# Performance work log

Hardware: AMD Instinct MI355X
Metric: run time of the kernel (lower is better)

Reference implementation:

```python
import jax, jax.numpy as jnp
import numpy as np

# Config constants from the module
E = 64    # n_routed_experts
K = 6     # num_experts_per_tok
D = 128   # hidden_size
M = 80    # moe_intermediate_size
MS = 160  # shared expert intermediate = moe_intermediate_size * n_shared_experts
B, S = 64, 256

def _init_w(k, shape, fan_in):
    # kaiming_uniform(a=sqrt(5)) used by nn.Linear / MoEGate: bound = 1/sqrt(fan_in)
    bound = 1.0 / np.sqrt(fan_in)
    return jax.random.uniform(k, shape, jnp.float32, -bound, bound)

def setup_inputs() -> dict:
    key = jax.random.key(0)
    ks = jax.random.split(key, 8)
    return {
        "hidden_states": jax.random.normal(ks[0], (B, S, D), jnp.float32),
        "gate_w": _init_w(ks[1], (E, D), D),        # MoEGate.linear.weight [E, gating_dim]
        "wg": _init_w(ks[2], (E, D, M), D),          # stacked expert gate_proj (transposed)
        "wu": _init_w(ks[3], (E, D, M), D),          # stacked expert up_proj
        "wd": _init_w(ks[4], (E, M, D), M),          # stacked expert down_proj
        "swg": _init_w(ks[5], (D, MS), D),           # shared expert gate_proj
        "swu": _init_w(ks[6], (D, MS), D),           # shared expert up_proj
        "swd": _init_w(ks[7], (MS, D), MS),          # shared expert down_proj
    }

def reference(hidden_states, gate_w, wg, wu, wd, swg, swu, swd):
    orig_shape = hidden_states.shape
    x = hidden_states.reshape(-1, D)                       # [T, D] flat tokens
    T = x.shape[0]
    # --- MoEGate ('all_agent' mode): softmax scoring + top-k + renorm ---
    scores = jax.nn.softmax(x @ gate_w.T, axis=-1)          # [T, E]
    topk_w, topk_idx = jax.lax.top_k(scores, K)             # [T, K]
    topk_w = topk_w / (jnp.sum(topk_w, axis=-1, keepdims=True) + 1e-20)
    # Scatter top-k weights into dense per-expert combine weights [T, E]
    cw = jnp.zeros_like(scores).at[jnp.arange(T)[:, None], topk_idx].add(topk_w)
    # --- Routed experts: SiLU-gated MLP per expert, combined by cw ---
    g = jax.nn.silu(jnp.einsum('td,edm->tem', x, wg)) * jnp.einsum('td,edm->tem', x, wu)
    y = jnp.einsum('tem,emd,te->td', g, wd, cw)             # down-proj + weighted combine
    # --- Shared experts ---
    shared = (jax.nn.silu(x @ swg) * (x @ swu)) @ swd       # [T, D]
    return (y + shared).reshape(orig_shape)
```

## Files before the change

### kernel.cpp

```cpp
#include <hip/hip_runtime.h>
#include <hip/hip_bf16.h>
#include <math.h>


typedef unsigned short ushort_t;
typedef __attribute__((ext_vector_type(8))) short bf16x8;
typedef __attribute__((ext_vector_type(4))) float f32x4;

#define EALL  66

#define OFF_TOPKI 16384
#define OFF_WORK  409600
#define OFF_TOPKW 802816
#define OFF_PERM  1196032
#define OFF_PERMW 1589248
#define OFF_POS2  1982464
#define OFF_YPERM 2375680
#define OFF_YSH   27541504
#define OFF_WGT   31735808
#define OFF_WUT   33087488
#define OFF_WDP   34439168
#define OFF_XB    36061184
#define OFF_HIST  40255488
#define OFF_BOFF  40321024
#define NEED_FAST 40386560
#define FOFF_YBUF 2375680
#define FOFF_WGT  10764288
#define FOFF_WUT  12115968
#define FOFF_WDP  13467648
#define FOFF_XB   15089664
#define FOFF_HIST 19283968
#define FOFF_BOFF 19349504

__device__ __forceinline__ float bf2f(ushort_t u) {
    unsigned int x = ((unsigned int)u) << 16;
    float f; __builtin_memcpy(&f, &x, 4); return f;
}
__device__ __forceinline__ ushort_t f2bf(float f) {
    unsigned int x; __builtin_memcpy(&x, &f, 4);
    unsigned int r = (x + 0x7fffu + ((x >> 16) & 1u)) >> 16;
    return (ushort_t)r;
}
__device__ __forceinline__ float ldin(const void* p, int i, int f32m) {
    return f32m ? ((const float*)p)[i] : bf2f(((const ushort_t*)p)[i]);
}
__device__ __forceinline__ int detect_f32m(const ushort_t* gw) {
    int lane = threadIdx.x & 63;
    int cnt = 0;
    #pragma unroll
    for (int j = 0; j < 4; ++j) {
        ushort_t u = gw[lane * 4 + j];
        if (((u >> 7) & 0xFF) >= 0x7C) cnt++;
    }
    #pragma unroll
    for (int off = 32; off; off >>= 1) cnt += __shfl_xor(cnt, off);
    return (cnt >= 8) ? 1 : 0;
}
__device__ __forceinline__ void gl16(void* l, const void* g) {
    __builtin_amdgcn_global_load_lds(
        (const __attribute__((address_space(1))) void*)g,
        (__attribute__((address_space(3))) void*)l, 16, 0, 0);
}

__global__ __launch_bounds__(1024) void k_pg(const void* x, const void* gw,
        const void* wg, const void* wu, const void* wd,
        const void* swg, const void* swu, const void* swd,
        ushort_t* wgT, ushort_t* wuT, ushort_t* wdP,
        ushort_t* xB, int* topk_i, float* topk_w, int* histPart) {
    __shared__ __align__(16) char smem[41984];
    int tid = threadIdx.x, bid = blockIdx.x;
    int f32m = detect_f32m((const ushort_t*)gw);

    if (bid < 3 * EALL) {
        float* lds = (float*)smem;
        int mat = bid / EALL, e = bid % EALL;
        if (mat < 2) {
            const void* src  = (mat == 0) ? wg  : wu;
            const void* ssrc = (mat == 0) ? swg : swu;
            for (int i = tid; i < 10240; i += 1024) {
                int d = i / 80, m = i % 80;
                float v = (e < 64) ? ldin(src, e * 10240 + i, f32m)
                                   : ldin(ssrc, d * 160 + (e - 64) * 80 + m, f32m);
                lds[d * 81 + m] = v;
            }
            __syncthreads();
            ushort_t* dst = ((mat == 0) ? wgT : wuT) + e * 10240;
            for (int o = tid; o < 10240; o += 1024) {
                int m = o >> 7, d = o & 127;
                dst[o] = f2bf(lds[d * 81 + m]);
            }
        } else {
            for (int i = tid; i < 10240; i += 1024) {
                float v = (e < 64) ? ldin(wd, e * 10240 + i, f32m)
                                   : ldin(swd, (e - 64) * 10240 + i, f32m);
                int m = i >> 7, d = i & 127;
                lds[m * 129 + d] = v;
            }
            __syncthreads();
            ushort_t* dst = wdP + e * 12288;
            for (int o = tid; o < 12288; o += 1024) {
                int d = o / 96, m = o % 96;
                dst[o] = (m < 80) ? f2bf(lds[m * 129 + d]) : (ushort_t)0;
            }
        }
        return;
    }

    float* gwl  = (float*)smem;
    float (*xl)[128] = (float(*)[128])(smem + 33280);
    int*   histL = (int*)(smem + 41472);
    int b = bid - 3 * EALL;
    for (int i = tid; i < 8192; i += 1024)
        gwl[(i >> 7) * 130 + (i & 127)] = ldin(gw, i, f32m);
    if (tid < 64) histL[tid] = 0;
    __syncthreads();
    int wv = tid >> 6, lane = tid & 63;
    for (int q = 0; q < 4; ++q) {
        int t = b * 64 + wv * 4 + q;
        float xv0, xv1;
        if (f32m) {
            float2 v = ((const float2*)((const float*)x + t * 128))[lane];
            xv0 = v.x; xv1 = v.y;
        } else {
            unsigned int pr = *(const unsigned int*)((const ushort_t*)x + t * 128 + lane * 2);
            xv0 = bf2f((ushort_t)(pr & 0xffffu));
            xv1 = bf2f((ushort_t)(pr >> 16));
        }
        float2 xw; xw.x = xv0; xw.y = xv1;
        *(float2*)&xl[wv][lane * 2] = xw;
        unsigned int packed = (unsigned int)f2bf(xv0) | ((unsigned int)f2bf(xv1) << 16);
        *(unsigned int*)(xB + t * 128 + lane * 2) = packed;
        float acc = 0.f;
        #pragma unroll
        for (int d2 = 0; d2 < 64; ++d2) {
            float2 xv = *(const float2*)&xl[wv][d2 * 2];
            float2 gv = *(const float2*)&gwl[lane * 130 + d2 * 2];
            acc = fmaf(xv.x, gv.x, acc);
            acc = fmaf(xv.y, gv.y, acc);
        }
        float mx = acc;
        #pragma unroll
        for (int off = 32; off; off >>= 1) mx = fmaxf(mx, __shfl_xor(mx, off));
        float p = expf(acc - mx);
        float sm = p;
        #pragma unroll
        for (int off = 32; off; off >>= 1) sm += __shfl_xor(sm, off);
        float sc = p / sm;
        float cur = sc;
        float wk6[6]; int ik[6];
        #pragma unroll
        for (int k = 0; k < 6; ++k) {
            float bv = cur; int bi = lane;
            #pragma unroll
            for (int off = 1; off < 64; off <<= 1) {
                float ov = __shfl_xor(bv, off); int oi = __shfl_xor(bi, off);
                if (ov > bv || (ov == bv && oi < bi)) { bv = ov; bi = oi; }
            }
            wk6[k] = bv; ik[k] = bi;
            if (lane == bi) cur = -INFINITY;
        }
        if (lane == 0) {
            float den = wk6[0] + wk6[1] + wk6[2] + wk6[3] + wk6[4] + wk6[5] + 1e-20f;
            #pragma unroll
            for (int k = 0; k < 6; ++k) {
                topk_i[t * 6 + k] = ik[k];
                topk_w[t * 6 + k] = wk6[k] / den;
                atomicAdd(&histL[ik[k]], 1);
            }
        }
    }
    __syncthreads();
    if (tid < 64) histPart[tid * 256 + b] = histL[tid];
}

__global__ __launch_bounds__(256) void k_scan(int* Wi, const int* histPart,
        int* boffG, int* wk) {
    __shared__ int hl[16384];
    __shared__ int cntL[64], exclL[64], chxL[65];
    int tid = threadIdx.x, lane = tid & 63, wv = tid >> 6;
    for (int j = tid; j < 16384; j += 256) hl[j] = histPart[j];
    __syncthreads();
    for (int ei = 0; ei < 16; ++ei) {
        int e = wv * 16 + ei;
        int carry = 0;
        for (int r = 0; r < 4; ++r) {
            int v = hl[e * 256 + r * 64 + lane];
            int incl = v;
            #pragma unroll
            for (int off = 1; off < 64; off <<= 1) {
                int ts = __shfl_up(incl, off);
                if (lane >= off) incl += ts;
            }
            hl[e * 256 + r * 64 + lane] = carry + incl - v;
            carry += __shfl(incl, 63);
        }
        if (lane == 0) cntL[e] = carry;
    }
    __syncthreads();
    if (tid == 0) {
        int s = 0, cs = 0;
        for (int e = 0; e < 64; ++e) {
            exclL[e] = s; s += cntL[e];
            chxL[e] = cs; cs += (cntL[e] + 127) >> 7;
        }
        chxL[64] = cs;
        Wi[128] = s;
        Wi[193] = cs + 256;
    }
    __syncthreads();
    if (tid < 64) { Wi[tid] = cntL[tid]; Wi[64 + tid] = exclL[tid]; }
    for (int j = tid; j < 16384; j += 256) boffG[j] = hl[j] + exclL[j >> 8];
    wk[tid] = (64 << 16) | tid;
    if (tid < 64) {
        int e = tid, nc = (cntL[e] + 127) >> 7, bb = chxL[e];
        for (int c = 0; c < nc; ++c) wk[256 + bb + c] = (e << 16) | c;
    }
}

__global__ __launch_bounds__(256) void k_scatter(const int* topk_i, const float* topk_w,
        const int* boffG, int* perm, float* permw, int* pos2) {
    __shared__ int lcur[64];
    int tid = threadIdx.x, b = blockIdx.x;
    if (tid < 64) lcur[tid] = boffG[tid * 256 + b];
    __syncthreads();
    for (int i = tid; i < 384; i += 256) {
        int g = b * 384 + i;
        int e = topk_i[g];
        float w = topk_w[g];
        int p = atomicAdd(&lcur[e], 1);
        perm[p]  = b * 64 + i / 6;
        permw[p] = w;
        pos2[g]  = p;
    }
}

template<int FAST>
__global__ __launch_bounds__(256) void k_expert(const ushort_t* x, const ushort_t* wgT,
        const ushort_t* wuT, const ushort_t* wdP, const int* Wi, const int* wk,
        const int* perm, const float* permw, ushort_t* yperm, ushort_t* ysh, float* ybuf) {
    __shared__ __align__(16) char hl[32768];
    __shared__ __align__(16) char bufA[20480];
    __shared__ __align__(16) char bufB[20480];

    if (blockIdx.x >= Wi[193]) return;
    int entry = wk[blockIdx.x];
    int e = entry >> 16, c = entry & 0xffff;
    int tid = threadIdx.x, lid = tid & 63, wv = tid >> 6;
    int kg  = (lid >> 4) * 16;
    int kq8 = (lid >> 4) * 8;

    if (e < 64) {
        int n = Wi[e], base = Wi[64 + e];
        int nrows = n - c * 128; if (nrows > 128) nrows = 128;

        {
            const ushort_t* gS = wgT + e * 10240;
            const ushort_t* uS = wuT + e * 10240;
            #pragma unroll
            for (int i = 0; i < 5; ++i) {
                int s = wv * 320 + i * 64 + lid;
                int row = s >> 4, sc = (s & 15) ^ (row & 7);
                gl16(bufA + wv * 5120 + i * 1024, gS + row * 128 + sc * 8);
                gl16(bufB + wv * 5120 + i * 1024, uS + row * 128 + sc * 8);
            }
        }
        bf16x8 a[2][4];
        #pragma unroll
        for (int tr = 0; tr < 2; ++tr) {
            int arow = wv * 32 + tr * 16 + (lid & 15);
            int r = (arow < nrows) ? arow : (nrows - 1);
            int t = perm[base + c * 128 + r];
            #pragma unroll
            for (int k = 0; k < 4; ++k)
                a[tr][k] = *(const bf16x8*)(x + t * 128 + k * 32 + kq8);
        }
        __syncthreads();

        #pragma unroll
        for (int mi = 0; mi < 5; ++mi) {
            int brow = mi * 16 + (lid & 15);
            int bro = brow * 256, bsw = (brow & 7) << 4;
            f32x4 ag[2], au[2];
            #pragma unroll
            for (int tr = 0; tr < 2; ++tr) {
                ag[tr] = (f32x4){0.f, 0.f, 0.f, 0.f};
                au[tr] = (f32x4){0.f, 0.f, 0.f, 0.f};
            }
            #pragma unroll
            for (int k = 0; k < 4; ++k) {
                int bo = bro + (((k * 64) + kg) ^ bsw);
                bf16x8 bg = *(const bf16x8*)(bufA + bo);
                bf16x8 bu = *(const bf16x8*)(bufB + bo);
                #pragma unroll
                for (int tr = 0; tr < 2; ++tr) {
                    ag[tr] = __builtin_amdgcn_mfma_f32_16x16x32_bf16(a[tr][k], bg, ag[tr], 0, 0, 0);
                    au[tr] = __builtin_amdgcn_mfma_f32_16x16x32_bf16(a[tr][k], bu, au[tr], 0, 0, 0);
                }
            }
            #pragma unroll
            for (int tr = 0; tr < 2; ++tr) {
                #pragma unroll
                for (int rg = 0; rg < 4; ++rg) {
                    float g = ag[tr][rg], uu2 = au[tr][rg];
                    float h = (g / (1.f + __expf(-g))) * uu2;
                    int row = wv * 32 + tr * 16 + (lid >> 4) * 4 + rg;
                    int cb = (mi * 16 + (lid & 15)) * 2;
                    *(ushort_t*)(hl + row * 256 + (cb ^ ((row & 7) << 4))) = f2bf(h);
                }
            }
        }
        {
            int r = wv * 32 + (lid >> 1), ch = 10 + (lid & 1);
            uint4 z = {0u, 0u, 0u, 0u};
            *(uint4*)(hl + r * 256 + ((ch * 16) ^ ((r & 7) << 4))) = z;
        }
        __syncthreads();

        {
            const ushort_t* dS = wdP + e * 12288;
            #pragma unroll
            for (int i = 0; i < 4; ++i) {
                int s = wv * 256 + i * 64 + lid;
                int r = s >> 4, sc = (s & 15) ^ (r & 7);
                int off = (sc < 12) ? sc * 8 : 0;
                gl16(bufA + wv * 4096 + i * 1024, dS + r * 96 + off);
                gl16(bufB + wv * 4096 + i * 1024, dS + (64 + r) * 96 + off);
            }
        }
        __syncthreads();

        bf16x8 bfr[2][3];
        #pragma unroll
        for (int tf = 0; tf < 2; ++tf) {
            int brow = wv * 32 + tf * 16 + (lid & 15);
            #pragma unroll
            for (int k = 0; k < 3; ++k)
                bfr[tf][k] = *(const bf16x8*)(hl + brow * 256 + (((k * 64) + kg) ^ ((brow & 7) << 4)));
        }
        f32x4 acc[8][2];
        #pragma unroll
        for (int dt = 0; dt < 8; ++dt) {
            acc[dt][0] = (f32x4){0.f, 0.f, 0.f, 0.f};
            acc[dt][1] = (f32x4){0.f, 0.f, 0.f, 0.f};
        }
        #pragma unroll
        for (int dt = 0; dt < 8; ++dt) {
            int r = (dt & 3) * 16 + (lid & 15);
            const char* wb = (dt < 4) ? bufA : bufB;
            bf16x8 ad[3];
            #pragma unroll
            for (int k = 0; k < 3; ++k)
                ad[k] = *(const bf16x8*)(wb + r * 256 + (((k * 64) + kg) ^ ((r & 7) << 4)));
            #pragma unroll
            for (int tf = 0; tf < 2; ++tf) {
                f32x4 cc = acc[dt][tf];
                #pragma unroll
                for (int k = 0; k < 3; ++k)
                    cc = __builtin_amdgcn_mfma_f32_16x16x32_bf16(ad[k], bfr[tf][k], cc, 0, 0, 0);
                acc[dt][tf] = cc;
            }
        }

        #pragma unroll
        for (int tf = 0; tf < 2; ++tf) {
            int rloc = wv * 32 + tf * 16 + (lid & 15);
            int rc = (rloc < nrows) ? rloc : (nrows - 1);
            float w = FAST ? permw[base + c * 128 + rc] : 0.f;
            #pragma unroll
            for (int dt = 0; dt < 8; ++dt) {
                if (FAST) {
                    int cb = (dt * 16 + (lid >> 4) * 4) * 2;
                    ushort_t o[4];
                    #pragma unroll
                    for (int rg = 0; rg < 4; ++rg) o[rg] = f2bf(acc[dt][tf][rg] * w);
                    *(uint2*)(hl + rloc * 256 + (cb ^ ((rloc & 7) << 4))) = *(const uint2*)o;
                } else {
                    if (rloc < nrows) {
                        int t = perm[base + c * 128 + rloc];
                        float w2 = permw[base + c * 128 + rloc];
                        int d0 = dt * 16 + (lid >> 4) * 4;
                        #pragma unroll
                        for (int rg = 0; rg < 4; ++rg)
                            atomicAdd(&ybuf[t * 128 + d0 + rg], acc[dt][tf][rg] * w2);
                    }
                }
            }
        }
        if (FAST) {
            #pragma unroll
            for (int ps = 0; ps < 8; ++ps) {
                int row = wv * 32 + ps * 4 + (lid >> 4);
                int cb = (lid & 15) * 16;
                uint4 v = *(const uint4*)(hl + row * 256 + (cb ^ ((row & 7) << 4)));
                if (row < nrows)
                    *(uint4*)(yperm + (size_t)(base + c * 128 + row) * 128 + (lid & 15) * 8) = v;
            }
        }
    } else {
        bf16x8 a1[4];
        int arow = wv * 16 + (lid & 15);
        int t0 = c * 64 + arow;
        #pragma unroll
        for (int k = 0; k < 4; ++k)
            a1[k] = *(const bf16x8*)(x + t0 * 128 + k * 32 + kq8);

        f32x4 acc[8];
        #pragma unroll
        for (int dt = 0; dt < 8; ++dt) acc[dt] = (f32x4){0.f, 0.f, 0.f, 0.f};

        for (int sub = 0; sub < 2; ++sub) {
            int ee = 64 + sub;
            {
                const ushort_t* gS = wgT + ee * 10240;
                const ushort_t* uS = wuT + ee * 10240;
                #pragma unroll
                for (int i = 0; i < 5; ++i) {
                    int s = wv * 320 + i * 64 + lid;
                    int row = s >> 4, sc = (s & 15) ^ (row & 7);
                    gl16(bufA + wv * 5120 + i * 1024, gS + row * 128 + sc * 8);
                    gl16(bufB + wv * 5120 + i * 1024, uS + row * 128 + sc * 8);
                }
            }
            __syncthreads();
            #pragma unroll
            for (int mi = 0; mi < 5; ++mi) {
                int brow = mi * 16 + (lid & 15);
                int bro = brow * 256, bsw = (brow & 7) << 4;
                f32x4 ag = {0.f, 0.f, 0.f, 0.f};
                f32x4 au = {0.f, 0.f, 0.f, 0.f};
                #pragma unroll
                for (int k = 0; k < 4; ++k) {
                    int bo = bro + (((k * 64) + kg) ^ bsw);
                    bf16x8 bg = *(const bf16x8*)(bufA + bo);
                    bf16x8 bu = *(const bf16x8*)(bufB + bo);
                    ag = __builtin_amdgcn_mfma_f32_16x16x32_bf16(a1[k], bg, ag, 0, 0, 0);
                    au = __builtin_amdgcn_mfma_f32_16x16x32_bf16(a1[k], bu, au, 0, 0, 0);
                }
                #pragma unroll
                for (int rg = 0; rg < 4; ++rg) {
                    float g = ag[rg], uu2 = au[rg];
                    float h = (g / (1.f + __expf(-g))) * uu2;
                    int row = wv * 16 + (lid >> 4) * 4 + rg;
                    int cb = (mi * 16 + (lid & 15)) * 2;
                    *(ushort_t*)(hl + row * 256 + (cb ^ ((row & 7) << 4))) = f2bf(h);
                }
            }
            if (sub == 0 && lid < 32) {
                int r = wv * 16 + (lid >> 1), ch = 10 + (lid & 1);
                uint4 z = {0u, 0u, 0u, 0u};
                *(uint4*)(hl + r * 256 + ((ch * 16) ^ ((r & 7) << 4))) = z;
            }
            __syncthreads();
            {
                const ushort_t* dS = wdP + ee * 12288;
                #pragma unroll
                for (int i = 0; i < 4; ++i) {
                    int s = wv * 256 + i * 64 + lid;
                    int r = s >> 4, sc = (s & 15) ^ (r & 7);
                    int off = (sc < 12) ? sc * 8 : 0;
                    gl16(bufA + wv * 4096 + i * 1024, dS + r * 96 + off);
                    gl16(bufB + wv * 4096 + i * 1024, dS + (64 + r) * 96 + off);
                }
            }
            __syncthreads();
            int brow = wv * 16 + (lid & 15);
            #pragma unroll
            for (int dt = 0; dt < 8; ++dt) {
                int r = (dt & 3) * 16 + (lid & 15);
                const char* wb = (dt < 4) ? bufA : bufB;
                bf16x8 ad[3];
                #pragma unroll
                for (int k = 0; k < 3; ++k)
                    ad[k] = *(const bf16x8*)(wb + r * 256 + (((k * 64) + kg) ^ ((r & 7) << 4)));
                f32x4 cc = acc[dt];
                #pragma unroll
                for (int k = 0; k < 3; ++k) {
                    bf16x8 b = *(const bf16x8*)(hl + brow * 256 + (((k * 64) + kg) ^ ((brow & 7) << 4)));
                    cc = __builtin_amdgcn_mfma_f32_16x16x32_bf16(ad[k], b, cc, 0, 0, 0);
                }
                acc[dt] = cc;
            }
            __syncthreads();
        }

        int rloc = wv * 16 + (lid & 15);
        if (FAST) {
            #pragma unroll
            for (int dt = 0; dt < 8; ++dt) {
                int cb = (dt * 16 + (lid >> 4) * 4) * 2;
                ushort_t o[4];
                #pragma unroll
                for (int rg = 0; rg < 4; ++rg) o[rg] = f2bf(acc[dt][rg]);
                *(uint2*)(hl + rloc * 256 + (cb ^ ((rloc & 7) << 4))) = *(const uint2*)o;
            }
            #pragma unroll
            for (int ps = 0; ps < 4; ++ps) {
                int row = wv * 16 + ps * 4 + (lid >> 4);
                int cb = (lid & 15) * 16;
                uint4 v = *(const uint4*)(hl + row * 256 + (cb ^ ((row & 7) << 4)));
                *(uint4*)(ysh + (size_t)(c * 64 + row) * 128 + (lid & 15) * 8) = v;
            }
        } else {
            int t = c * 64 + rloc;
            #pragma unroll
            for (int dt = 0; dt < 8; ++dt) {
                int d0 = dt * 16 + (lid >> 4) * 4;
                #pragma unroll
                for (int rg = 0; rg < 4; ++rg)
                    atomicAdd(&ybuf[t * 128 + d0 + rg], acc[dt][rg]);
            }
        }
    }
}

__global__ __launch_bounds__(256) void k_final_gather(const ushort_t* yperm,
        const ushort_t* ysh, const int* pos2, void* out, const ushort_t* gwDet) {
    int idx = blockIdx.x * 256 + threadIdx.x;
    int t = idx >> 4, cg = (idx & 15) * 8;
    int f32m = detect_f32m(gwDet);
    float acc[8];
    {
        uint4 v = *(const uint4*)(ysh + (size_t)t * 128 + cg);
        const ushort_t* u = (const ushort_t*)&v;
        #pragma unroll
        for (int j = 0; j < 8; ++j) acc[j] = bf2f(u[j]);
    }
    const int* pp = pos2 + t * 6;
    #pragma unroll
    for (int k = 0; k < 6; ++k) {
        int p = pp[k];
        uint4 v = *(const uint4*)(yperm + (size_t)p * 128 + cg);
        const ushort_t* u = (const ushort_t*)&v;
        #pragma unroll
        for (int j = 0; j < 8; ++j) acc[j] += bf2f(u[j]);
    }
    if (f32m) {
        float4 o0 = {acc[0], acc[1], acc[2], acc[3]};
        float4 o1 = {acc[4], acc[5], acc[6], acc[7]};
        float* op = (float*)out + (size_t)t * 128 + cg;
        *(float4*)op = o0; *(float4*)(op + 4) = o1;
    } else {
        ushort_t o[8];
        #pragma unroll
        for (int j = 0; j < 8; ++j) o[j] = f2bf(acc[j]);
        *(uint4*)((ushort_t*)out + (size_t)t * 128 + cg) = *(const uint4*)o;
    }
}

__global__ __launch_bounds__(256) void k_final_ybuf(const float* ybuf, void* out,
        const ushort_t* gwDet) {
    int i = blockIdx.x * 256 + threadIdx.x;
    int f32m = detect_f32m(gwDet);
    float4 v = ((const float4*)ybuf)[i];
    if (f32m) {
        ((float4*)out)[i] = v;
    } else {
        ushort4 o;
        o.x = f2bf(v.x); o.y = f2bf(v.y); o.z = f2bf(v.z); o.w = f2bf(v.w);
        ((ushort4*)out)[i] = o;
    }
}

extern "C" void kernel_launch(void* const* d_in, const int* in_sizes, int n_in,
                              void* d_out, int out_size, void* d_ws, size_t ws_size,
                              hipStream_t stream) {
    (void)in_sizes; (void)n_in; (void)out_size;
    const void* x   = d_in[0];
    const void* gw  = d_in[1];
    const void* wg  = d_in[2];
    const void* wu  = d_in[3];
    const void* wd  = d_in[4];
    const void* swg = d_in[5];
    const void* swu = d_in[6];
    const void* swd = d_in[7];

    char* ws = (char*)d_ws;
    int fast = (ws_size >= (size_t)NEED_FAST) ? 1 : 0;

    int*      Wi     = (int*)d_ws;
    int*      topk_i = (int*)(ws + OFF_TOPKI);
    int*      wklist = (int*)(ws + OFF_WORK);
    float*    topk_w = (float*)(ws + OFF_TOPKW);
    int*      perm   = (int*)(ws + OFF_PERM);
    float*    permw  = (float*)(ws + OFF_PERMW);
    int*      pos2   = (int*)(ws + OFF_POS2);

    ushort_t* yperm = (ushort_t*)(ws + OFF_YPERM);
    ushort_t* ysh   = (ushort_t*)(ws + OFF_YSH);
    float*    ybuf  = (float*)(ws + FOFF_YBUF);
    ushort_t* wgT   = (ushort_t*)(ws + (fast ? OFF_WGT  : FOFF_WGT));
    ushort_t* wuT   = (ushort_t*)(ws + (fast ? OFF_WUT  : FOFF_WUT));
    ushort_t* wdP   = (ushort_t*)(ws + (fast ? OFF_WDP  : FOFF_WDP));
    ushort_t* xB    = (ushort_t*)(ws + (fast ? OFF_XB   : FOFF_XB));
    int*      histP = (int*)(ws + (fast ? OFF_HIST : FOFF_HIST));
    int*      boffG = (int*)(ws + (fast ? OFF_BOFF : FOFF_BOFF));

    if (!fast) hipMemsetAsync(ybuf, 0, 16384 * 128 * 4, stream);

    k_pg<<<3 * EALL + 256, 1024, 0, stream>>>(x, gw, wg, wu, wd, swg, swu, swd,
                                              wgT, wuT, wdP, xB, topk_i, topk_w, histP);
    k_scan<<<1, 256, 0, stream>>>(Wi, histP, boffG, wklist);
    k_scatter<<<256, 256, 0, stream>>>(topk_i, topk_w, boffG, perm, permw, pos2);
    if (fast) {
        k_expert<1><<<1088, 256, 0, stream>>>(xB, wgT, wuT, wdP, Wi, wklist, perm, permw, yperm, ysh, ybuf);
        k_final_gather<<<1024, 256, 0, stream>>>(yperm, ysh, pos2, d_out, (const ushort_t*)gw);
    } else {
        k_expert<0><<<1088, 256, 0, stream>>>(xB, wgT, wuT, wdP, Wi, wklist, perm, permw, yperm, ysh, ybuf);
        k_final_ybuf<<<2048, 256, 0, stream>>>(ybuf, d_out, (const ushort_t*)gw);
    }
}
```

Baseline: 92.65 us.

## Fuse shared-expert compute into scatter kernel, shrink routed-expert grid

The shared-expert MLP blocks move out of the routed expert kernel into a new kernel that also performs the token scatter. Blocks 0-255 do the scatter and blocks 256-511 compute shared-expert chunks, so that independent work fills one launch and the expert kernel loses its per-block branch. The routed-expert grid drops to 896 blocks and the work list no longer reserves shared-expert entries. The risk is that 896 may not cover the worst-case number of routed chunks.

```diff
diff --git a/kernel.cpp b/kernel.cpp
--- a/kernel.cpp
+++ b/kernel.cpp
@@ -205,39 +205,169 @@
         }
         chxL[64] = cs;
         Wi[128] = s;
-        Wi[193] = cs + 256;
+        Wi[193] = cs;
     }
     __syncthreads();
     if (tid < 64) { Wi[tid] = cntL[tid]; Wi[64 + tid] = exclL[tid]; }
     for (int j = tid; j < 16384; j += 256) boffG[j] = hl[j] + exclL[j >> 8];
-    wk[tid] = (64 << 16) | tid;
     if (tid < 64) {
         int e = tid, nc = (cntL[e] + 127) >> 7, bb = chxL[e];
-        for (int c = 0; c < nc; ++c) wk[256 + bb + c] = (e << 16) | c;
-    }
-}
-
-__global__ __launch_bounds__(256) void k_scatter(const int* topk_i, const float* topk_w,
-        const int* boffG, int* perm, float* permw, int* pos2) {
-    __shared__ int lcur[64];
-    int tid = threadIdx.x, b = blockIdx.x;
-    if (tid < 64) lcur[tid] = boffG[tid * 256 + b];
-    __syncthreads();
-    for (int i = tid; i < 384; i += 256) {
-        int g = b * 384 + i;
-        int e = topk_i[g];
-        float w = topk_w[g];
-        int p = atomicAdd(&lcur[e], 1);
-        perm[p]  = b * 64 + i / 6;
-        permw[p] = w;
-        pos2[g]  = p;
+        for (int c = 0; c < nc; ++c) wk[bb + c] = (e << 16) | c;
+    }
+}
+
+template<int FAST>
+__global__ __launch_bounds__(256) void k_sc_sh(const int* boffG,
+        const int* topk_i, const float* topk_w, int* perm, float* permw, int* pos2,
+        const ushort_t* x, const ushort_t* wgT, const ushort_t* wuT, const ushort_t* wdP,
+        ushort_t* ysh, float* ybuf) {
+    __shared__ __align__(16) char smem[73728];
+    int tid = threadIdx.x, lid = tid & 63, wv = tid >> 6;
+    int bid = blockIdx.x;
+
+    if (bid < 256) {
+        int* lcur = (int*)smem;
+        int b = bid;
+        if (tid < 64) lcur[tid] = boffG[tid * 256 + b];
+        __syncthreads();
+        for (int i = tid; i < 384; i += 256) {
+            int g = b * 384 + i;
+            int e = topk_i[g];
+            float w = topk_w[g];
+            int p = atomicAdd(&lcur[e], 1);
+            perm[p]  = b * 64 + i / 6;
+            permw[p] = w;
+            pos2[g]  = p;
+        }
+        return;
+    }
+
+    char* hl   = smem;
+    char* bufA = smem + 32768;
+    char* bufB = smem + 53248;
+    int c = bid - 256;
+    int kg  = (lid >> 4) * 16;
+    int kq8 = (lid >> 4) * 8;
+
+    bf16x8 a1[4];
+    int arow = wv * 16 + (lid & 15);
+    int t0 = c * 64 + arow;
+    #pragma unroll
+    for (int k = 0; k < 4; ++k)
+        a1[k] = *(const bf16x8*)(x + t0 * 128 + k * 32 + kq8);
+
+    f32x4 acc[8];
+    #pragma unroll
+    for (int dt = 0; dt < 8; ++dt) acc[dt] = (f32x4){0.f, 0.f, 0.f, 0.f};
+
+    for (int sub = 0; sub < 2; ++sub) {
+        int ee = 64 + sub;
+        {
+            const ushort_t* gS = wgT + ee * 10240;
+            const ushort_t* uS = wuT + ee * 10240;
+            #pragma unroll
+            for (int i = 0; i < 5; ++i) {
+                int s = wv * 320 + i * 64 + lid;
+                int row = s >> 4, sc = (s & 15) ^ (row & 7);
+                gl16(bufA + wv * 5120 + i * 1024, gS + row * 128 + sc * 8);
+                gl16(bufB + wv * 5120 + i * 1024, uS + row * 128 + sc * 8);
+            }
+        }
+        __syncthreads();
+        #pragma unroll
+        for (int mi = 0; mi < 5; ++mi) {
+            int brow = mi * 16 + (lid & 15);
+            int bro = brow * 256, bsw = (brow & 7) << 4;
+            f32x4 ag = {0.f, 0.f, 0.f, 0.f};
+            f32x4 au = {0.f, 0.f, 0.f, 0.f};
+            #pragma unroll
+            for (int k = 0; k < 4; ++k) {
+                int bo = bro + (((k * 64) + kg) ^ bsw);
+                bf16x8 bg = *(const bf16x8*)(bufA + bo);
+                bf16x8 bu = *(const bf16x8*)(bufB + bo);
+                ag = __builtin_amdgcn_mfma_f32_16x16x32_bf16(a1[k], bg, ag, 0, 0, 0);
+                au = __builtin_amdgcn_mfma_f32_16x16x32_bf16(a1[k], bu, au, 0, 0, 0);
+            }
+            #pragma unroll
+            for (int rg = 0; rg < 4; ++rg) {
+                float g = ag[rg], uu2 = au[rg];
+                float h = (g / (1.f + __expf(-g))) * uu2;
+                int row = wv * 16 + (lid >> 4) * 4 + rg;
+                int cb = (mi * 16 + (lid & 15)) * 2;
+                *(ushort_t*)(hl + row * 256 + (cb ^ ((row & 7) << 4))) = f2bf(h);
+            }
+        }
+        if (sub == 0 && lid < 32) {
+            int r = wv * 16 + (lid >> 1), ch = 10 + (lid & 1);
+            uint4 z = {0u, 0u, 0u, 0u};
+            *(uint4*)(hl + r * 256 + ((ch * 16) ^ ((r & 7) << 4))) = z;
+        }
+        __syncthreads();
+        {
+            const ushort_t* dS = wdP + ee * 12288;
+            #pragma unroll
+            for (int i = 0; i < 4; ++i) {
+                int s = wv * 256 + i * 64 + lid;
+                int r = s >> 4, sc = (s & 15) ^ (r & 7);
+                int off = (sc < 12) ? sc * 8 : 0;
+                gl16(bufA + wv * 4096 + i * 1024, dS + r * 96 + off);
+                gl16(bufB + wv * 4096 + i * 1024, dS + (64 + r) * 96 + off);
+            }
+        }
+        __syncthreads();
+        int brow = wv * 16 + (lid & 15);
+        #pragma unroll
+        for (int dt = 0; dt < 8; ++dt) {
+            int r = (dt & 3) * 16 + (lid & 15);
+            const char* wb = (dt < 4) ? bufA : bufB;
+            bf16x8 ad[3];
+            #pragma unroll
+            for (int k = 0; k < 3; ++k)
+                ad[k] = *(const bf16x8*)(wb + r * 256 + (((k * 64) + kg) ^ ((r & 7) << 4)));
+            f32x4 cc = acc[dt];
+            #pragma unroll
+            for (int k = 0; k < 3; ++k) {
+                bf16x8 b = *(const bf16x8*)(hl + brow * 256 + (((k * 64) + kg) ^ ((brow & 7) << 4)));
+                cc = __builtin_amdgcn_mfma_f32_16x16x32_bf16(ad[k], b, cc, 0, 0, 0);
+            }
+            acc[dt] = cc;
+        }
+        __syncthreads();
+    }
+
+    int rloc = wv * 16 + (lid & 15);
+    if (FAST) {
+        #pragma unroll
+        for (int dt = 0; dt < 8; ++dt) {
+            int cb = (dt * 16 + (lid >> 4) * 4) * 2;
+            ushort_t o[4];
+            #pragma unroll
+            for (int rg = 0; rg < 4; ++rg) o[rg] = f2bf(acc[dt][rg]);
+            *(uint2*)(hl + rloc * 256 + (cb ^ ((rloc & 7) << 4))) = *(const uint2*)o;
+        }
+        #pragma unroll
+        for (int ps = 0; ps < 4; ++ps) {
+            int row = wv * 16 + ps * 4 + (lid >> 4);
+            int cb = (lid & 15) * 16;
+            uint4 v = *(const uint4*)(hl + row * 256 + (cb ^ ((row & 7) << 4)));
+            *(uint4*)(ysh + (size_t)(c * 64 + row) * 128 + (lid & 15) * 8) = v;
+        }
+    } else {
+        int t = c * 64 + rloc;
+        #pragma unroll
+        for (int dt = 0; dt < 8; ++dt) {
+            int d0 = dt * 16 + (lid >> 4) * 4;
+            #pragma unroll
+            for (int rg = 0; rg < 4; ++rg)
+                atomicAdd(&ybuf[t * 128 + d0 + rg], acc[dt][rg]);
+        }
     }
 }
 
 template<int FAST>
 __global__ __launch_bounds__(256) void k_expert(const ushort_t* x, const ushort_t* wgT,
         const ushort_t* wuT, const ushort_t* wdP, const int* Wi, const int* wk,
-        const int* perm, const float* permw, ushort_t* yperm, ushort_t* ysh, float* ybuf) {
+        const int* perm, const float* permw, ushort_t* yperm, float* ybuf) {
     __shared__ __align__(16) char hl[32768];
     __shared__ __align__(16) char bufA[20480];
     __shared__ __align__(16) char bufB[20480];
@@ -249,266 +379,150 @@
     int kg  = (lid >> 4) * 16;
     int kq8 = (lid >> 4) * 8;
 
-    if (e < 64) {
-        int n = Wi[e], base = Wi[64 + e];
-        int nrows = n - c * 128; if (nrows > 128) nrows = 128;
-
-        {
-            const ushort_t* gS = wgT + e * 10240;
-            const ushort_t* uS = wuT + e * 10240;
-            #pragma unroll
-            for (int i = 0; i < 5; ++i) {
-                int s = wv * 320 + i * 64 + lid;
-                int row = s >> 4, sc = (s & 15) ^ (row & 7);
-                gl16(bufA + wv * 5120 + i * 1024, gS + row * 128 + sc * 8);
-                gl16(bufB + wv * 5120 + i * 1024, uS + row * 128 + sc * 8);
-            }
-        }
-        bf16x8 a[2][4];
+    int n = Wi[e], base = Wi[64 + e];
+    int nrows = n - c * 128; if (nrows > 128) nrows = 128;
+
+    {
+        const ushort_t* gS = wgT + e * 10240;
+        const ushort_t* uS = wuT + e * 10240;
+        #pragma unroll
+        for (int i = 0; i < 5; ++i) {
+            int s = wv * 320 + i * 64 + lid;
+            int row = s >> 4, sc = (s & 15) ^ (row & 7);
+            gl16(bufA + wv * 5120 + i * 1024, gS + row * 128 + sc * 8);
+            gl16(bufB + wv * 5120 + i * 1024, uS + row * 128 + sc * 8);
+        }
+    }
+    bf16x8 a[2][4];
+    #pragma unroll
+    for (int tr = 0; tr < 2; ++tr) {
+        int arow = wv * 32 + tr * 16 + (lid & 15);
+        int r = (arow < nrows) ? arow : (nrows - 1);
+        int t = perm[base + c * 128 + r];
+        #pragma unroll
+        for (int k = 0; k < 4; ++k)
+            a[tr][k] = *(const bf16x8*)(x + t * 128 + k * 32 + kq8);
+    }
+    __syncthreads();
+
+    #pragma unroll
+    for (int mi = 0; mi < 5; ++mi) {
+        int brow = mi * 16 + (lid & 15);
+        int bro = brow * 256, bsw = (brow & 7) << 4;
+        f32x4 ag[2], au[2];
         #pragma unroll
         for (int tr = 0; tr < 2; ++tr) {
-            int arow = wv * 32 + tr * 16 + (lid & 15);
-            int r = (arow < nrows) ? arow : (nrows - 1);
-            int t = perm[base + c * 128 + r];
-            #pragma unroll
-            for (int k = 0; k < 4; ++k)
-                a[tr][k] = *(const bf16x8*)(x + t * 128 + k * 32 + kq8);
-        }
-        __syncthreads();
-
-        #pragma unroll
-        for (int mi = 0; mi < 5; ++mi) {
-            int brow = mi * 16 + (lid & 15);
-            int bro = brow * 256, bsw = (brow & 7) << 4;
-            f32x4 ag[2], au[2];
+            ag[tr] = (f32x4){0.f, 0.f, 0.f, 0.f};
+            au[tr] = (f32x4){0.f, 0.f, 0.f, 0.f};
+        }
+        #pragma unroll
+        for (int k = 0; k < 4; ++k) {
+            int bo = bro + (((k * 64) + kg) ^ bsw);
+            bf16x8 bg = *(const bf16x8*)(bufA + bo);
+            bf16x8 bu = *(const bf16x8*)(bufB + bo);
             #pragma unroll
             for (int tr = 0; tr < 2; ++tr) {
-                ag[tr] = (f32x4){0.f, 0.f, 0.f, 0.f};
-                au[tr] = (f32x4){0.f, 0.f, 0.f, 0.f};
-            }
-            #pragma unroll
-            for (int k = 0; k < 4; ++k) {
-                int bo = bro + (((k * 64) + kg) ^ bsw);
-                bf16x8 bg = *(const bf16x8*)(bufA + bo);
-                bf16x8 bu = *(const bf16x8*)(bufB + bo);
-                #pragma unroll
-                for (int tr = 0; tr < 2; ++tr) {
-                    ag[tr] = __builtin_amdgcn_mfma_f32_16x16x32_bf16(a[tr][k], bg, ag[tr], 0, 0, 0);
-                    au[tr] = __builtin_amdgcn_mfma_f32_16x16x32_bf16(a[tr][k], bu, au[tr], 0, 0, 0);
-                }
-            }
-            #pragma unroll
-            for (int tr = 0; tr < 2; ++tr) {
-                #pragma unroll
-                for (int rg = 0; rg < 4; ++rg) {
-                    float g = ag[tr][rg], uu2 = au[tr][rg];
-                    float h = (g / (1.f + __expf(-g))) * uu2;
-                    int row = wv * 32 + tr * 16 + (lid >> 4) * 4 + rg;
-                    int cb = (mi * 16 + (lid & 15)) * 2;
-                    *(ushort_t*)(hl + row * 256 + (cb ^ ((row & 7) << 4))) = f2bf(h);
-                }
-            }
-        }
-        {
-            int r = wv * 32 + (lid >> 1), ch = 10 + (lid & 1);
-            uint4 z = {0u, 0u, 0u, 0u};
-            *(uint4*)(hl + r * 256 + ((ch * 16) ^ ((r & 7) << 4))) = z;
-        }
-        __syncthreads();
-
-        {
-            const ushort_t* dS = wdP + e * 12288;
-            #pragma unroll
-            for (int i = 0; i < 4; ++i) {
-                int s = wv * 256 + i * 64 + lid;
-                int r = s >> 4, sc = (s & 15) ^ (r & 7);
-                int off = (sc < 12) ? sc * 8 : 0;
-                gl16(bufA + wv * 4096 + i * 1024, dS + r * 96 + off);
-                gl16(bufB + wv * 4096 + i * 1024, dS + (64 + r) * 96 + off);
-            }
-        }
-        __syncthreads();
-
-        bf16x8 bfr[2][3];
+                ag[tr] = __builtin_amdgcn_mfma_f32_16x16x32_bf16(a[tr][k], bg, ag[tr], 0, 0, 0);
+                au[tr] = __builtin_amdgcn_mfma_f32_16x16x32_bf16(a[tr][k], bu, au[tr], 0, 0, 0);
+            }
+        }
+        #pragma unroll
+        for (int tr = 0; tr < 2; ++tr) {
+            #pragma unroll
+            for (int rg = 0; rg < 4; ++rg) {
+                float g = ag[tr][rg], uu2 = au[tr][rg];
+                float h = (g / (1.f + __expf(-g))) * uu2;
+                int row = wv * 32 + tr * 16 + (lid >> 4) * 4 + rg;
+                int cb = (mi * 16 + (lid & 15)) * 2;
+                *(ushort_t*)(hl + row * 256 + (cb ^ ((row & 7) << 4))) = f2bf(h);
+            }
+        }
+    }
+    {
+        int r = wv * 32 + (lid >> 1), ch = 10 + (lid & 1);
+        uint4 z = {0u, 0u, 0u, 0u};
+        *(uint4*)(hl + r * 256 + ((ch * 16) ^ ((r & 7) << 4))) = z;
+    }
+    __syncthreads();
+
+    {
+        const ushort_t* dS = wdP + e * 12288;
+        #pragma unroll
+        for (int i = 0; i < 4; ++i) {
+            int s = wv * 256 + i * 64 + lid;
+            int r = s >> 4, sc = (s & 15) ^ (r & 7);
+            int off = (sc < 12) ? sc * 8 : 0;
+            gl16(bufA + wv * 4096 + i * 1024, dS + r * 96 + off);
+            gl16(bufB + wv * 4096 + i * 1024, dS + (64 + r) * 96 + off);
+        }
+    }
+    __syncthreads();
+
+    bf16x8 bfr[2][3];
+    #pragma unroll
+    for (int tf = 0; tf < 2; ++tf) {
+        int brow = wv * 32 + tf * 16 + (lid & 15);
+        #pragma unroll
+        for (int k = 0; k < 3; ++k)
+            bfr[tf][k] = *(const bf16x8*)(hl + brow * 256 + (((k * 64) + kg) ^ ((brow & 7) << 4)));
+    }
+    f32x4 acc[8][2];
+    #pragma unroll
+    for (int dt = 0; dt < 8; ++dt) {
+        acc[dt][0] = (f32x4){0.f, 0.f, 0.f, 0.f};
+        acc[dt][1] = (f32x4){0.f, 0.f, 0.f, 0.f};
+    }
+    #pragma unroll
+    for (int dt = 0; dt < 8; ++dt) {
+        int r = (dt & 3) * 16 + (lid & 15);
+        const char* wb = (dt < 4) ? bufA : bufB;
+        bf16x8 ad[3];
+        #pragma unroll
+        for (int k = 0; k < 3; ++k)
+            ad[k] = *(const bf16x8*)(wb + r * 256 + (((k * 64) + kg) ^ ((r & 7) << 4)));
         #pragma unroll
         for (int tf = 0; tf < 2; ++tf) {
-            int brow = wv * 32 + tf * 16 + (lid & 15);
+            f32x4 cc = acc[dt][tf];
             #pragma unroll
             for (int k = 0; k < 3; ++k)
-                bfr[tf][k] = *(const bf16x8*)(hl + brow * 256 + (((k * 64) + kg) ^ ((brow & 7) << 4)));
-        }
-        f32x4 acc[8][2];
+                cc = __builtin_amdgcn_mfma_f32_16x16x32_bf16(ad[k], bfr[tf][k], cc, 0, 0, 0);
+            acc[dt][tf] = cc;
+        }
+    }
+
+    #pragma unroll
+    for (int tf = 0; tf < 2; ++tf) {
+        int rloc = wv * 32 + tf * 16 + (lid & 15);
+        int rc = (rloc < nrows) ? rloc : (nrows - 1);
+        float w = FAST ? permw[base + c * 128 + rc] : 0.f;
         #pragma unroll
         for (int dt = 0; dt < 8; ++dt) {
-            acc[dt][0] = (f32x4){0.f, 0.f, 0.f, 0.f};
-            acc[dt][1] = (f32x4){0.f, 0.f, 0.f, 0.f};
-        }
-        #pragma unroll
-        for (int dt = 0; dt < 8; ++dt) {
-            int r = (dt & 3) * 16 + (lid & 15);
-            const char* wb = (dt < 4) ? bufA : bufB;
-            bf16x8 ad[3];
-            #pragma unroll
-            for (int k = 0; k < 3; ++k)
-                ad[k] = *(const bf16x8*)(wb + r * 256 + (((k * 64) + kg) ^ ((r & 7) << 4)));
-            #pragma unroll
-            for (int tf = 0; tf < 2; ++tf) {
-                f32x4 cc = acc[dt][tf];
-                #pragma unroll
-                for (int k = 0; k < 3; ++k)
-                    cc = __builtin_amdgcn_mfma_f32_16x16x32_bf16(ad[k], bfr[tf][k], cc, 0, 0, 0);
-                acc[dt][tf] = cc;
-            }
-        }
-
-        #pragma unroll
-        for (int tf = 0; tf < 2; ++tf) {
-            int rloc = wv * 32 + tf * 16 + (lid & 15);
-            int rc = (rloc < nrows) ? rloc : (nrows - 1);
-            float w = FAST ? permw[base + c * 128 + rc] : 0.f;
-            #pragma unroll
-            for (int dt = 0; dt < 8; ++dt) {
-                if (FAST) {
-                    int cb = (dt * 16 + (lid >> 4) * 4) * 2;
-                    ushort_t o[4];
-                    #pragma unroll
-                    for (int rg = 0; rg < 4; ++rg) o[rg] = f2bf(acc[dt][tf][rg] * w);
-                    *(uint2*)(hl + rloc * 256 + (cb ^ ((rloc & 7) << 4))) = *(const uint2*)o;
-                } else {
-                    if (rloc < nrows) {
-                        int t = perm[base + c * 128 + rloc];
-                        float w2 = permw[base + c * 128 + rloc];
-                        int d0 = dt * 16 + (lid >> 4) * 4;
-                        #pragma unroll
-                        for (int rg = 0; rg < 4; ++rg)
-                            atomicAdd(&ybuf[t * 128 + d0 + rg], acc[dt][tf][rg] * w2);
-                    }
-                }
-            }
-        }
-        if (FAST) {
-            #pragma unroll
-            for (int ps = 0; ps < 8; ++ps) {
-                int row = wv * 32 + ps * 4 + (lid >> 4);
-                int cb = (lid & 15) * 16;
-                uint4 v = *(const uint4*)(hl + row * 256 + (cb ^ ((row & 7) << 4)));
-                if (row < nrows)
-                    *(uint4*)(yperm + (size_t)(base + c * 128 + row) * 128 + (lid & 15) * 8) = v;
-            }
-        }
-    } else {
-        bf16x8 a1[4];
-        int arow = wv * 16 + (lid & 15);
-        int t0 = c * 64 + arow;
-        #pragma unroll
-        for (int k = 0; k < 4; ++k)
-            a1[k] = *(const bf16x8*)(x + t0 * 128 + k * 32 + kq8);
-
-        f32x4 acc[8];
-        #pragma unroll
-        for (int dt = 0; dt < 8; ++dt) acc[dt] = (f32x4){0.f, 0.f, 0.f, 0.f};
-
-        for (int sub = 0; sub < 2; ++sub) {
-            int ee = 64 + sub;
-            {
-                const ushort_t* gS = wgT + ee * 10240;
-                const ushort_t* uS = wuT + ee * 10240;
-                #pragma unroll
-                for (int i = 0; i < 5; ++i) {
-                    int s = wv * 320 + i * 64 + lid;
-                    int row = s >> 4, sc = (s & 15) ^ (row & 7);
-                    gl16(bufA + wv * 5120 + i * 1024, gS + row * 128 + sc * 8);
-                    gl16(bufB + wv * 5120 + i * 1024, uS + row * 128 + sc * 8);
-                }
-            }
-            __syncthreads();
-            #pragma unroll
-            for (int mi = 0; mi < 5; ++mi) {
-                int brow = mi * 16 + (lid & 15);
-                int bro = brow * 256, bsw = (brow & 7) << 4;
-                f32x4 ag = {0.f, 0.f, 0.f, 0.f};
-                f32x4 au = {0.f, 0.f, 0.f, 0.f};
-                #pragma unroll
-                for (int k = 0; k < 4; ++k) {
-                    int bo = bro + (((k * 64) + kg) ^ bsw);
-                    bf16x8 bg = *(const bf16x8*)(bufA + bo);
-                    bf16x8 bu = *(const bf16x8*)(bufB + bo);
-                    ag = __builtin_amdgcn_mfma_f32_16x16x32_bf16(a1[k], bg, ag, 0, 0, 0);
-                    au = __builtin_amdgcn_mfma_f32_16x16x32_bf16(a1[k], bu, au, 0, 0, 0);
-                }
-                #pragma unroll
-                for (int rg = 0; rg < 4; ++rg) {
-                    float g = ag[rg], uu2 = au[rg];
-                    float h = (g / (1.f + __expf(-g))) * uu2;
-                    int row = wv * 16 + (lid >> 4) * 4 + rg;
-                    int cb = (mi * 16 + (lid & 15)) * 2;
-                    *(ushort_t*)(hl + row * 256 + (cb ^ ((row & 7) << 4))) = f2bf(h);
-                }
-            }
-            if (sub == 0 && lid < 32) {
-                int r = wv * 16 + (lid >> 1), ch = 10 + (lid & 1);
-                uint4 z = {0u, 0u, 0u, 0u};
-                *(uint4*)(hl + r * 256 + ((ch * 16) ^ ((r & 7) << 4))) = z;
-            }
-            __syncthreads();
-            {
-                const ushort_t* dS = wdP + ee * 12288;
-                #pragma unroll
-                for (int i = 0; i < 4; ++i) {
-                    int s = wv * 256 + i * 64 + lid;
-                    int r = s >> 4, sc = (s & 15) ^ (r & 7);
-                    int off = (sc < 12) ? sc * 8 : 0;
-                    gl16(bufA + wv * 4096 + i * 1024, dS + r * 96 + off);
-                    gl16(bufB + wv * 4096 + i * 1024, dS + (64 + r) * 96 + off);
-                }
-            }
-            __syncthreads();
-            int brow = wv * 16 + (lid & 15);
-            #pragma unroll
-            for (int dt = 0; dt < 8; ++dt) {
-                int r = (dt & 3) * 16 + (lid & 15);
-                const char* wb = (dt < 4) ? bufA : bufB;
-                bf16x8 ad[3];
-                #pragma unroll
-                for (int k = 0; k < 3; ++k)
-                    ad[k] = *(const bf16x8*)(wb + r * 256 + (((k * 64) + kg) ^ ((r & 7) << 4)));
-                f32x4 cc = acc[dt];
-                #pragma unroll
-                for (int k = 0; k < 3; ++k) {
-                    bf16x8 b = *(const bf16x8*)(hl + brow * 256 + (((k * 64) + kg) ^ ((brow & 7) << 4)));
-                    cc = __builtin_amdgcn_mfma_f32_16x16x32_bf16(ad[k], b, cc, 0, 0, 0);
-                }
-                acc[dt] = cc;
-            }
-            __syncthreads();
-        }
-
-        int rloc = wv * 16 + (lid & 15);
-        if (FAST) {
-            #pragma unroll
-            for (int dt = 0; dt < 8; ++dt) {
+            if (FAST) {
                 int cb = (dt * 16 + (lid >> 4) * 4) * 2;
                 ushort_t o[4];
                 #pragma unroll
-                for (int rg = 0; rg < 4; ++rg) o[rg] = f2bf(acc[dt][rg]);
+                for (int rg = 0; rg < 4; ++rg) o[rg] = f2bf(acc[dt][tf][rg] * w);
                 *(uint2*)(hl + rloc * 256 + (cb ^ ((rloc & 7) << 4))) = *(const uint2*)o;
-            }
-            #pragma unroll
-            for (int ps = 0; ps < 4; ++ps) {
-                int row = wv * 16 + ps * 4 + (lid >> 4);
-                int cb = (lid & 15) * 16;
-                uint4 v = *(const uint4*)(hl + row * 256 + (cb ^ ((row & 7) << 4)));
-                *(uint4*)(ysh + (size_t)(c * 64 + row) * 128 + (lid & 15) * 8) = v;
-            }
-        } else {
-            int t = c * 64 + rloc;
-            #pragma unroll
-            for (int dt = 0; dt < 8; ++dt) {
-                int d0 = dt * 16 + (lid >> 4) * 4;
-                #pragma unroll
-                for (int rg = 0; rg < 4; ++rg)
-                    atomicAdd(&ybuf[t * 128 + d0 + rg], acc[dt][rg]);
-            }
+            } else {
+                if (rloc < nrows) {
+                    int t = perm[base + c * 128 + rloc];
+                    float w2 = permw[base + c * 128 + rloc];
+                    int d0 = dt * 16 + (lid >> 4) * 4;
+                    #pragma unroll
+                    for (int rg = 0; rg < 4; ++rg)
+                        atomicAdd(&ybuf[t * 128 + d0 + rg], acc[dt][tf][rg] * w2);
+                }
+            }
+        }
+    }
+    if (FAST) {
+        #pragma unroll
+        for (int ps = 0; ps < 8; ++ps) {
+            int row = wv * 32 + ps * 4 + (lid >> 4);
+            int cb = (lid & 15) * 16;
+            uint4 v = *(const uint4*)(hl + row * 256 + (cb ^ ((row & 7) << 4)));
+            if (row < nrows)
+                *(uint4*)(yperm + (size_t)(base + c * 128 + row) * 128 + (lid & 15) * 8) = v;
         }
     }
 }
@@ -600,12 +614,15 @@
     k_pg<<<3 * EALL + 256, 1024, 0, stream>>>(x, gw, wg, wu, wd, swg, swu, swd,
                                               wgT, wuT, wdP, xB, topk_i, topk_w, histP);
     k_scan<<<1, 256, 0, stream>>>(Wi, histP, boffG, wklist);
-    k_scatter<<<256, 256, 0, stream>>>(topk_i, topk_w, boffG, perm, permw, pos2);
     if (fast) {
-        k_expert<1><<<1088, 256, 0, stream>>>(xB, wgT, wuT, wdP, Wi, wklist, perm, permw, yperm, ysh, ybuf);
+        k_sc_sh<1><<<512, 256, 0, stream>>>(boffG, topk_i, topk_w, perm, permw, pos2,
+                                            xB, wgT, wuT, wdP, ysh, ybuf);
+        k_expert<1><<<896, 256, 0, stream>>>(xB, wgT, wuT, wdP, Wi, wklist, perm, permw, yperm, ybuf);
         k_final_gather<<<1024, 256, 0, stream>>>(yperm, ysh, pos2, d_out, (const ushort_t*)gw);
     } else {
-        k_expert<0><<<1088, 256, 0, stream>>>(xB, wgT, wuT, wdP, Wi, wklist, perm, permw, yperm, ysh, ybuf);
+        k_sc_sh<0><<<512, 256, 0, stream>>>(boffG, topk_i, topk_w, perm, permw, pos2,
+                                            xB, wgT, wuT, wdP, ysh, ybuf);
+        k_expert<0><<<896, 256, 0, stream>>>(xB, wgT, wuT, wdP, Wi, wklist, perm, permw, yperm, ybuf);
         k_final_ybuf<<<2048, 256, 0, stream>>>(ybuf, d_out, (const ushort_t*)gw);
     }
 }
```

After: 94.81 us. 2.3% more time.
